# Kernel optimization log

Measured on AMD Instinct MI355X. Metric: run time of the kernel, lower is better.

The kernel has to match this reference:

```python
import jax, jax.numpy as jnp
import numpy as np

DIM = 1024; H = 16; KVH = 4; HD = 64          # head_dim = DIM // H
I = 2048                                       # intermediate_size = 2*DIM
N = 16                                         # ssm_state_size
DTR = 64                                       # dt_rank = DIM // 16
K = 4                                          # conv kernel
BASE = 10000.0
EPS = 1.1920929e-07                            # torch F.rms_norm default eps (fp32 finfo eps)

def rms_norm(x):
    return x * jax.lax.rsqrt(jnp.mean(x * x, axis=-1, keepdims=True) + EPS)

def rope_tables(S, dims):
    inv = 1.0 / BASE ** (jnp.arange(0, dims, 2, dtype=jnp.float32) / dims)
    f = jnp.outer(jnp.arange(S, dtype=jnp.float32), inv)   # [S, dims//2]
    return jnp.cos(f), jnp.sin(f)

def apply_rope(x, cos, sin):
    half = x.shape[-1] // 2
    x1, x2 = x[..., :half], x[..., half:]
    return jnp.concatenate([x1 * cos + x2 * sin, -x1 * sin + x2 * cos], axis=-1)

def setup_inputs() -> dict:
    key = jax.random.key(0)
    ks = jax.random.split(key, 12)
    B, S = 2, 2048
    def w(k, shape, s=0.02):
        return jax.random.normal(k, shape, jnp.float32) * s
    return {
        "x": jax.random.normal(ks[0], (B, S, DIM), jnp.float32),
        "W_mamba": w(ks[1], (2 * I, DIM)),
        "W_q": w(ks[2], (DIM, DIM)),
        "W_kv": w(ks[3], (2 * KVH * HD, DIM)),
        "q_gain": jnp.full((H,), 1.0, jnp.float32),
        "conv_w": w(ks[4], (I, K), 0.2),
        "conv_b": jnp.zeros((I,), jnp.float32),
        "W_xproj": w(ks[5], (DTR + 2 * N, I)),
        "W_dt": w(ks[6], (I, DTR)),
        "b_dt": w(ks[7], (I,), 0.5),
        "A_log": jnp.log(jnp.broadcast_to(jnp.arange(1, N + 1, dtype=jnp.float32), (I, N))),
        "D": jnp.ones((I,), jnp.float32),
        "W_mamba_out": w(ks[8], (DIM, I)),
        "W_proj": w(ks[9], (DIM, DIM)),
        "merge_alpha": jnp.zeros((1,), jnp.float32),
    }

def reference(x, W_mamba, W_q, W_kv, q_gain, conv_w, conv_b, W_xproj, W_dt, b_dt,
              A_log, D, W_mamba_out, W_proj, merge_alpha):
    B, S, _ = x.shape
    # --- parallel input projection for the mamba branch ---
    mp = x @ W_mamba.T                         # [B,S,2I]
    x_ssm, gate = mp[..., :I], mp[..., I:]
    # --- attention branch (GQA + full RoPE + per-head q gain) ---
    q = (x @ W_q.T).reshape(B, S, H, HD).transpose(0, 2, 1, 3)
    kv = x @ W_kv.T
    k = kv[..., :KVH * HD].reshape(B, S, KVH, HD).transpose(0, 2, 1, 3)
    v = kv[..., KVH * HD:].reshape(B, S, KVH, HD).transpose(0, 2, 1, 3)
    q = rms_norm(q); k = rms_norm(k)
    cos, sin = rope_tables(S, HD)
    q = apply_rope(q, cos, sin)
    k = apply_rope(k, cos, sin)
    q = q * q_gain[None, :, None, None]
    nrep = H // KVH
    k = jnp.repeat(k, nrep, axis=1)
    v = jnp.repeat(v, nrep, axis=1)
    scores = jnp.einsum('bhqd,bhkd->bhqk', q, k) / jnp.sqrt(jnp.float32(HD))
    mask = jnp.tril(jnp.ones((S, S), bool))
    scores = jnp.where(mask, scores, -jnp.inf)
    y = jnp.einsum('bhqk,bhkd->bhqd', jax.nn.softmax(scores, axis=-1), v)
    attn_out = y.transpose(0, 2, 1, 3).reshape(B, S, DIM)
    # --- mamba/SSM branch: causal depthwise conv1d + silu ---
    xc = x_ssm.transpose(0, 2, 1)              # [B,I,S]
    u = jax.lax.conv_general_dilated(xc, conv_w[:, None, :], (1,), [(K - 1, 0)],
                                     dimension_numbers=('NCH', 'OIH', 'NCH'),
                                     feature_group_count=I) + conv_b[None, :, None]
    u = u * jax.nn.sigmoid(u)                  # silu, [B,I,S]
    u_bsi = u.transpose(0, 2, 1)               # [B,S,I]
    params = u_bsi @ W_xproj.T                 # [B,S,DTR+2N]
    dt_low = params[..., :DTR]
    Bm = params[..., DTR:DTR + N]
    Cm = params[..., DTR + N:]
    delta = jax.nn.softplus(dt_low @ W_dt.T + b_dt)   # [B,S,I] (delta_bias + softplus)
    A = -jnp.exp(A_log)                        # [I,N]
    def step(state, inp):
        d_t, b_t, c_t, u_t = inp               # [B,I],[B,N],[B,N],[B,I]
        dA = jnp.exp(d_t[:, :, None] * A[None])
        state = state * dA + d_t[:, :, None] * b_t[:, None, :] * u_t[:, :, None]
        y_t = jnp.sum(state * c_t[:, None, :], axis=-1)
        return state, y_t
    xs = (delta.transpose(1, 0, 2), Bm.transpose(1, 0, 2),
          Cm.transpose(1, 0, 2), u_bsi.transpose(1, 0, 2))
    state0 = jnp.zeros((B, I, N), x.dtype)
    _, ys = jax.lax.scan(step, state0, xs)     # ys: [S,B,I]
    y_ssm = ys.transpose(1, 0, 2) + u_bsi * D  # + D skip
    y_ssm = y_ssm * (gate * jax.nn.sigmoid(gate))      # gated by silu(z)
    mamba_out = y_ssm @ W_mamba_out.T          # [B,S,DIM]
    # --- gated merge + output projection ---
    alpha = jax.nn.sigmoid(merge_alpha)
    merged = alpha * attn_out + (1.0 - alpha) * mamba_out
    return merged @ W_proj.T
```

## Files before the change

kernel.cpp:

```cpp
#include <hip/hip_runtime.h>
#include <hip/hip_bf16.h>

#define B_   2
#define S_   2048
#define T_   4096
#define DIM_ 1024
#define H_   16
#define KVH_ 4
#define HD_  64
#define I_   2048
#define N_   16
#define DTR_ 64
#define MB   ((size_t)1 << 20)

typedef __hip_bfloat16 bf16;
typedef __attribute__((ext_vector_type(8))) short short8;
typedef __attribute__((ext_vector_type(4))) short short4v;
typedef __attribute__((ext_vector_type(4))) float f32x4;

__device__ __forceinline__ float b2f(bf16 v){ return __bfloat162float(v); }
__device__ __forceinline__ bf16  f2b(float v){ return __float2bfloat16(v); }
__device__ __forceinline__ float s2f(short s){
  return __builtin_bit_cast(float, ((unsigned int)(unsigned short)s) << 16);
}
__device__ __forceinline__ short f2s(float v){
  return (short)__builtin_bit_cast(unsigned short, f2b(v));
}

__device__ __forceinline__ void async16(const void* g, void* l) {
  __builtin_amdgcn_global_load_lds((__attribute__((address_space(1))) void*)g,
                                   (__attribute__((address_space(3))) void*)l, 16, 0, 0);
}

__global__ __launch_bounds__(256)
void cast_f2b(const float* __restrict__ in, bf16* __restrict__ out, int n4)
{
  const int i = blockIdx.x * 256 + threadIdx.x;
  if (i >= n4) return;
  const float4 v = ((const float4*)in)[i];
  short4v o;
  o.x = f2s(v.x); o.y = f2s(v.y); o.z = f2s(v.z); o.w = f2s(v.w);
  *(short4v*)(out + (size_t)i * 4) = o;
}

template<int MODE, int TS>
__global__ __launch_bounds__(256)
void gemm_nt(const bf16* __restrict__ A, int lda,
             const bf16* __restrict__ W, int ldw,
             void* __restrict__ C, int ldc,
             bf16* __restrict__ Ct, int ldt,
             const float* __restrict__ bias,
             int M, int N, int K)
{
  __shared__ __align__(16) bf16 As[128*32];
  __shared__ __align__(16) bf16 Bs[128*32];
  const int tid  = threadIdx.x;
  const int lane = tid & 63;
  const int wave = tid >> 6;
  const int l16  = lane & 15;
  const int quad = lane >> 4;
  const int wm   = (wave >> 1) << 6;
  const int wn   = (wave & 1) << 6;
  const int m0   = blockIdx.x << 7;
  const int n0   = blockIdx.y << 7;

  f32x4 acc[4][4];
  const f32x4 zero = {0.f, 0.f, 0.f, 0.f};
  #pragma unroll
  for (int i = 0; i < 4; i++)
    #pragma unroll
    for (int j = 0; j < 4; j++) acc[i][j] = zero;

  for (int k0 = 0; k0 < K; k0 += 32) {
    #pragma unroll
    for (int p = 0; p < 2; p++) {
      const int linear = ((p << 8) + tid) << 4;
      const int row    = linear >> 6;
      const int inrow  = linear & 63;
      async16(A + (size_t)(m0 + row) * lda + k0 + (inrow >> 1), (char*)As + linear);
      int wr = n0 + row; if (wr > N - 1) wr = N - 1;
      async16(W + (size_t)wr * ldw + k0 + (inrow >> 1), (char*)Bs + linear);
    }
    __syncthreads();
    short8 af[4], bfr[4];
    #pragma unroll
    for (int mt = 0; mt < 4; mt++)
      af[mt] = *(const short8*)((const char*)As + ((wm + (mt << 4) + l16) << 6) + (quad << 4));
    #pragma unroll
    for (int nt = 0; nt < 4; nt++)
      bfr[nt] = *(const short8*)((const char*)Bs + ((wn + (nt << 4) + l16) << 6) + (quad << 4));
    #pragma unroll
    for (int mt = 0; mt < 4; mt++)
      #pragma unroll
      for (int nt = 0; nt < 4; nt++)
        acc[mt][nt] = __builtin_amdgcn_mfma_f32_16x16x32_bf16(af[mt], bfr[nt], acc[mt][nt], 0, 0, 0);
    __syncthreads();
  }

  #pragma unroll
  for (int mt = 0; mt < 4; mt++) {
    #pragma unroll
    for (int nt = 0; nt < 4; nt++) {
      const int col = n0 + wn + (nt << 4) + l16;
      if (col >= N) continue;
      const int rowbase = m0 + wm + (mt << 4) + (quad << 2);
      float v[4];
      #pragma unroll
      for (int r = 0; r < 4; r++) {
        float t = acc[mt][nt][r];
        if (MODE == 2) {
          t += bias[col];
          t = (t > 20.f) ? t : log1pf(__expf(t));
        }
        v[r] = t;
      }
      if (TS == 0 || TS == 2) {
        #pragma unroll
        for (int r = 0; r < 4; r++) {
          if (MODE == 0) ((float*)C)[(size_t)(rowbase + r) * ldc + col] = v[r];
          else           ((bf16*)C)[(size_t)(rowbase + r) * ldc + col] = f2b(v[r]);
        }
      }
      if (TS >= 1) {
        short4v p;
        #pragma unroll
        for (int r = 0; r < 4; r++) p[r] = f2s(v[r]);
        *(short4v*)(Ct + (size_t)col * ldt + rowbase) = p;
      }
    }
  }
}

__global__ __launch_bounds__(256)
void qkv_prep(const bf16* __restrict__ qraw, const bf16* __restrict__ kvraw,
              const float* __restrict__ q_gain,
              bf16* __restrict__ qn, bf16* __restrict__ kn, bf16* __restrict__ vt)
{
  const int wid  = blockIdx.x * 4 + (threadIdx.x >> 6);
  const int lane = threadIdx.x & 63;
  const int t    = wid / 24;
  const int slot = wid % 24;
  const int b = t >> 11, s = t & 2047;

  float val;
  if (slot < 16)       val = b2f(qraw [(size_t)t * 1024 + slot * 64 + lane]);
  else if (slot < 20)  val = b2f(kvraw[(size_t)t * 512  + (slot - 16) * 64 + lane]);
  else                 val = b2f(kvraw[(size_t)t * 512  + 256 + (slot - 20) * 64 + lane]);

  if (slot < 20) {
    float ss = val * val;
    #pragma unroll
    for (int off = 32; off; off >>= 1) ss += __shfl_xor(ss, off);
    val *= rsqrtf(ss * (1.0f / 64.0f) + 1.1920929e-07f);
    const int j = lane & 31;
    const float x1 = __shfl(val, j);
    const float x2 = __shfl(val, j + 32);
    const float inv = powf(10000.0f, -(float)j * (1.0f / 32.0f));
    const float ang = (float)s * inv;
    const float c = cosf(ang), sn = sinf(ang);
    val = (lane < 32) ? (x1 * c + x2 * sn) : (x2 * c - x1 * sn);
  }
  if (slot < 16) {
    val *= q_gain[slot];
    qn[((size_t)(b * 16 + slot) * 2048 + s) * 64 + lane] = f2b(val);
  } else if (slot < 20) {
    kn[((size_t)(b * 4 + (slot - 16)) * 2048 + s) * 64 + lane] = f2b(val);
  } else {
    vt[((size_t)(b * 4 + (slot - 20)) * 64 + lane) * 2048 + s] = f2b(val);
  }
}

__global__ __launch_bounds__(64)
void attn_fwd(const bf16* __restrict__ qn, const bf16* __restrict__ kn,
              const bf16* __restrict__ vt, bf16* __restrict__ attn)
{
  __shared__ __align__(16) bf16 Plds[16][72];
  const int b = blockIdx.z, h = blockIdx.y;
  const int lane = threadIdx.x;
  const int l16 = lane & 15, quad = lane >> 4;
  const int q0 = (127 - blockIdx.x) * 16;
  const int kvh = h >> 2;
  const bf16* Q  = qn + (size_t)(b * 16 + h)  * 2048 * 64;
  const bf16* Kp = kn + (size_t)(b * 4 + kvh) * 2048 * 64;
  const bf16* Vt = vt + (size_t)(b * 4 + kvh) * 64 * 2048;

  const short8 qf0 = *(const short8*)(Q + (size_t)(q0 + l16) * 64 + quad * 8);
  const short8 qf1 = *(const short8*)(Q + (size_t)(q0 + l16) * 64 + 32 + quad * 8);

  f32x4 acc[4];
  const f32x4 zero = {0.f, 0.f, 0.f, 0.f};
  #pragma unroll
  for (int i = 0; i < 4; i++) acc[i] = zero;
  float m_r[4], l_r[4];
  #pragma unroll
  for (int r = 0; r < 4; r++) { m_r[r] = -1e30f; l_r[r] = 0.f; }

  const int kend = q0 + 16;
  for (int kb = 0; kb < kend; kb += 64) {
    f32x4 s[4];
    #pragma unroll
    for (int t = 0; t < 4; t++) {
      const bf16* kr = Kp + (size_t)(kb + t * 16 + l16) * 64;
      const short8 kf0 = *(const short8*)(kr + quad * 8);
      const short8 kf1 = *(const short8*)(kr + 32 + quad * 8);
      f32x4 sv = zero;
      sv = __builtin_amdgcn_mfma_f32_16x16x32_bf16(qf0, kf0, sv, 0, 0, 0);
      sv = __builtin_amdgcn_mfma_f32_16x16x32_bf16(qf1, kf1, sv, 0, 0, 0);
      s[t] = sv;
    }
    float alpha[4], p[4][4];
    #pragma unroll
    for (int r = 0; r < 4; r++) {
      const int row = q0 + quad * 4 + r;
      float v[4];
      #pragma unroll
      for (int t = 0; t < 4; t++) {
        float x = s[t][r] * 0.125f;
        if (kb + t * 16 + l16 > row) x = -1e30f;
        v[t] = x;
      }
      float tm = fmaxf(fmaxf(v[0], v[1]), fmaxf(v[2], v[3]));
      tm = fmaxf(tm, __shfl_xor(tm, 1)); tm = fmaxf(tm, __shfl_xor(tm, 2));
      tm = fmaxf(tm, __shfl_xor(tm, 4)); tm = fmaxf(tm, __shfl_xor(tm, 8));
      const float nm = fmaxf(m_r[r], tm);
      alpha[r] = __expf(m_r[r] - nm);
      m_r[r] = nm;
      float ps = 0.f;
      #pragma unroll
      for (int t = 0; t < 4; t++) { p[r][t] = __expf(v[t] - nm); ps += p[r][t]; }
      ps += __shfl_xor(ps, 1); ps += __shfl_xor(ps, 2);
      ps += __shfl_xor(ps, 4); ps += __shfl_xor(ps, 8);
      l_r[r] = l_r[r] * alpha[r] + ps;
    }
    #pragma unroll
    for (int nt = 0; nt < 4; nt++)
      #pragma unroll
      for (int r = 0; r < 4; r++) acc[nt][r] *= alpha[r];

    #pragma unroll
    for (int r = 0; r < 4; r++)
      #pragma unroll
      for (int t = 0; t < 4; t++)
        Plds[quad * 4 + r][t * 16 + l16] = f2b(p[r][t]);

    #pragma unroll
    for (int c = 0; c < 2; c++) {
      const short8 pf = *(const short8*)(&Plds[l16][c * 32 + quad * 8]);
      #pragma unroll
      for (int nt = 0; nt < 4; nt++) {
        const short8 vf = *(const short8*)(Vt + (size_t)(nt * 16 + l16) * 2048 + kb + c * 32 + quad * 8);
        acc[nt] = __builtin_amdgcn_mfma_f32_16x16x32_bf16(pf, vf, acc[nt], 0, 0, 0);
      }
    }
  }

  #pragma unroll
  for (int nt = 0; nt < 4; nt++)
    #pragma unroll
    for (int r = 0; r < 4; r++) {
      const int row = q0 + quad * 4 + r;
      attn[((size_t)b * 2048 + row) * 1024 + h * 64 + nt * 16 + l16] = f2b(acc[nt][r] / l_r[r]);
    }
}

__global__ __launch_bounds__(256)
void conv_silu_t(const bf16* __restrict__ xssmT, const float* __restrict__ cw,
                 const float* __restrict__ cb, bf16* __restrict__ uT)
{
  const int i = blockIdx.x;
  const int t = blockIdx.y * 256 + threadIdx.x;
  const int s = t & 2047;
  float acc = cb[i];
  #pragma unroll
  for (int kk = 0; kk < 4; kk++) {
    if (s - 3 + kk >= 0)
      acc += s2f(__builtin_bit_cast(short, xssmT[(size_t)i * 4096 + t - 3 + kk])) * cw[i * 4 + kk];
  }
  const float sig = 1.f / (1.f + __expf(-acc));
  uT[(size_t)i * 4096 + t] = f2b(acc * sig);
}

__global__ __launch_bounds__(256)
void transpose_bf16(const bf16* __restrict__ in, bf16* __restrict__ out,
                    int R, int C)
{
  __shared__ bf16 tile[64][65];
  const int c0 = blockIdx.x * 64, r0 = blockIdx.y * 64;
  #pragma unroll
  for (int it = 0; it < 2; it++) {
    const int linear = (it * 256 + threadIdx.x) * 8;
    const int r = linear >> 6, cc = linear & 63;
    const short8 v = *(const short8*)(in + (size_t)(r0 + r) * C + c0 + cc);
    #pragma unroll
    for (int k = 0; k < 8; k++)
      tile[r][cc + k] = __builtin_bit_cast(bf16, (unsigned short)v[k]);
  }
  __syncthreads();
  #pragma unroll
  for (int it = 0; it < 2; it++) {
    const int linear = (it * 256 + threadIdx.x) * 8;
    const int oc = linear >> 6, k = linear & 63;
    short8 v;
    #pragma unroll
    for (int kk = 0; kk < 8; kk++)
      v[kk] = (short)__builtin_bit_cast(unsigned short, tile[k + kk][oc]);
    *(short8*)(out + (size_t)(c0 + oc) * R + r0 + k) = v;
  }
}

__global__ __launch_bounds__(256)
void finish_y(const bf16* __restrict__ yT, const bf16* __restrict__ gT,
              bf16* __restrict__ out)
{
  __shared__ bf16 tile[64][65];
  const int t0 = blockIdx.x * 64, i0 = blockIdx.y * 64;
  #pragma unroll
  for (int it = 0; it < 2; it++) {
    const int linear = (it * 256 + threadIdx.x) * 8;
    const int r = linear >> 6, cc = linear & 63;
    const size_t off = (size_t)(i0 + r) * 4096 + t0 + cc;
    const short8 y8 = *(const short8*)(yT + off);
    const short8 g8 = *(const short8*)(gT + off);
    #pragma unroll
    for (int k = 0; k < 8; k++) {
      const float g  = s2f(g8[k]);
      const float gs = g / (1.f + __expf(-g));
      tile[r][cc + k] = f2b(s2f(y8[k]) * gs);
    }
  }
  __syncthreads();
  #pragma unroll
  for (int it = 0; it < 2; it++) {
    const int linear = (it * 256 + threadIdx.x) * 8;
    const int oc = linear >> 6, k = linear & 63;
    short8 v;
    #pragma unroll
    for (int kk = 0; kk < 8; kk++)
      v[kk] = (short)__builtin_bit_cast(unsigned short, tile[k + kk][oc]);
    *(short8*)(out + (size_t)(t0 + oc) * 2048 + i0 + k) = v;
  }
}

__global__ __launch_bounds__(256)
void ssm_scan(const bf16* __restrict__ dltT, const bf16* __restrict__ uT,
              const bf16* __restrict__ prmT, const float* __restrict__ A_log,
              const float* __restrict__ Dv, bf16* __restrict__ youtT)
{
  __shared__ float Pl[16][17], Fl[16][17], Il[16][17];
  const int blk = blockIdx.x;
  const int b = blk >> 11, i = blk & 2047;
  const int n = threadIdx.x & 15, c = threadIdx.x >> 4;
  const float a  = -__expf(A_log[i * 16 + n]);
  const float Di = Dv[i];
  const size_t rowoff = (size_t)b * 2048 + c * 128;
  const bf16* dp = dltT  + (size_t)i * 4096 + rowoff;
  const bf16* up = uT    + (size_t)i * 4096 + rowoff;
  const bf16* Bp = prmT  + (size_t)(64 + n) * 4096 + rowoff;
  const bf16* Cp = prmT  + (size_t)(80 + n) * 4096 + rowoff;
  bf16*       yp = youtT + (size_t)i * 4096 + rowoff;

  float P = 1.f, F = 0.f;
  for (int j0 = 0; j0 < 128; j0 += 8) {
    const short8 d8 = *(const short8*)(dp + j0);
    const short8 u8 = *(const short8*)(up + j0);
    const short8 B8 = *(const short8*)(Bp + j0);
    #pragma unroll
    for (int j = 0; j < 8; j++) {
      const float dt = s2f(d8[j]);
      const float dA = __expf(dt * a);
      P *= dA;
      F = F * dA + dt * s2f(u8[j]) * s2f(B8[j]);
    }
  }
  Pl[n][c] = P; Fl[n][c] = F;
  __syncthreads();

  if (threadIdx.x < 16) {
    const int nn = threadIdx.x;
    float s = 0.f;
    #pragma unroll
    for (int cc = 0; cc < 16; cc++) {
      Il[nn][cc] = s;
      s = Fl[nn][cc] + Pl[nn][cc] * s;
    }
  }
  __syncthreads();

  float state = Il[n][c];
  for (int j0 = 0; j0 < 128; j0 += 8) {
    const short8 d8 = *(const short8*)(dp + j0);
    const short8 u8 = *(const short8*)(up + j0);
    const short8 B8 = *(const short8*)(Bp + j0);
    const short8 C8 = *(const short8*)(Cp + j0);
    short8 o8;
    #pragma unroll
    for (int j = 0; j < 8; j++) {
      const float dt = s2f(d8[j]);
      const float ut = s2f(u8[j]);
      const float dA = __expf(dt * a);
      state = state * dA + dt * ut * s2f(B8[j]);
      float y = state * s2f(C8[j]);
      y += __shfl_xor(y, 1); y += __shfl_xor(y, 2);
      y += __shfl_xor(y, 4); y += __shfl_xor(y, 8);
      o8[j] = f2s(y + ut * Di);
    }
    if (n == 0) *(short8*)(yp + j0) = o8;
  }
}

__global__ __launch_bounds__(256)
void merge_k(const bf16* __restrict__ attn, const bf16* __restrict__ mamba,
             const float* __restrict__ malpha, bf16* __restrict__ merged)
{
  const size_t idx = (size_t)blockIdx.x * 256 + threadIdx.x;
  const float al = 1.f / (1.f + __expf(-malpha[0]));
  merged[idx] = f2b(al * b2f(attn[idx]) + (1.f - al) * b2f(mamba[idx]));
}

extern "C" void kernel_launch(void* const* d_in, const int* in_sizes, int n_in,
                              void* d_out, int out_size, void* d_ws, size_t ws_size,
                              hipStream_t stream)
{
  const float* x_f     = (const float*)d_in[0];
  const float* Wm_f    = (const float*)d_in[1];
  const float* Wq_f    = (const float*)d_in[2];
  const float* Wkv_f   = (const float*)d_in[3];
  const float* q_gain  = (const float*)d_in[4];
  const float* conv_w  = (const float*)d_in[5];
  const float* conv_b  = (const float*)d_in[6];
  const float* Wxp_f   = (const float*)d_in[7];
  const float* Wdt_f   = (const float*)d_in[8];
  const float* b_dt    = (const float*)d_in[9];
  const float* A_log   = (const float*)d_in[10];
  const float* Dv      = (const float*)d_in[11];
  const float* Wmo_f   = (const float*)d_in[12];
  const float* Wp_f    = (const float*)d_in[13];
  const float* malpha  = (const float*)d_in[14];

  char* wp = (char*)d_ws;
  bf16*  xb    = (bf16*)(wp + 0 * MB);
  bf16*  Wm_b  = (bf16*)(wp + 8 * MB);
  bf16*  Wq_b  = (bf16*)(wp + 16 * MB);
  bf16*  Wkv_b = (bf16*)(wp + 18 * MB);
  bf16*  xssmT = (bf16*)(wp + 19 * MB);
  bf16*  gateT = (bf16*)(wp + 35 * MB);
  bf16*  u     = (bf16*)(wp + 51 * MB);
  bf16*  uT    = (bf16*)(wp + 67 * MB);
  bf16*  qraw  = (bf16*)(wp + 83 * MB);
  bf16*  kvraw = (bf16*)(wp + 91 * MB);
  bf16*  dltT  = (bf16*)(wp + 95 * MB);
  bf16*  qn    = (bf16*)(wp + 0 * MB);
  bf16*  kn    = (bf16*)(wp + 8 * MB);
  bf16*  vtb   = (bf16*)(wp + 10 * MB);
  bf16*  Wxp_b = (bf16*)(wp + 12 * MB);
  bf16*  Wdt_b = (bf16*)(wp + 12 * MB + 512 * 1024);
  bf16*  prm   = (bf16*)(wp + 13 * MB);
  bf16*  prmT  = (bf16*)(wp + 13 * MB + 768 * 1024);
  bf16*  Wp_b  = (bf16*)(wp + 16 * MB);
  bf16*  attnb = (bf16*)(wp + 83 * MB);
  bf16*  Wmo_b = (bf16*)(wp + 91 * MB);
  bf16*  ybuf  = (bf16*)(wp + 19 * MB);
  bf16*  ybufT = (bf16*)(wp + 51 * MB);
  bf16*  mam   = (bf16*)(wp + 35 * MB);
  bf16*  mrg   = (bf16*)(wp + 43 * MB);
  (void)ws_size; (void)in_sizes; (void)n_in; (void)out_size;

  auto cast = [&](const float* src, bf16* dst, int n) {
    const int n4 = n >> 2;
    cast_f2b<<<dim3((n4 + 255) / 256), 256, 0, stream>>>(src, dst, n4);
  };
  cast(x_f,   xb,    T_ * 1024);
  cast(Wm_f,  Wm_b,  4096 * 1024);
  cast(Wq_f,  Wq_b,  1024 * 1024);
  cast(Wkv_f, Wkv_b, 512 * 1024);

  gemm_nt<1,1><<<dim3(32, 16), 256, 0, stream>>>(xb, 1024, Wm_b,               1024, nullptr, 0, xssmT, 4096, nullptr, T_, 2048, 1024);
  gemm_nt<1,1><<<dim3(32, 16), 256, 0, stream>>>(xb, 1024, Wm_b + 2048 * 1024, 1024, nullptr, 0, gateT, 4096, nullptr, T_, 2048, 1024);
  gemm_nt<1,0><<<dim3(32, 8),  256, 0, stream>>>(xb, 1024, Wq_b,  1024, qraw,  1024, nullptr, 0, nullptr, T_, 1024, 1024);
  gemm_nt<1,0><<<dim3(32, 4),  256, 0, stream>>>(xb, 1024, Wkv_b, 1024, kvraw,  512, nullptr, 0, nullptr, T_,  512, 1024);

  qkv_prep<<<dim3((T_ * 24) / 4), 256, 0, stream>>>(qraw, kvraw, q_gain, qn, kn, vtb);
  conv_silu_t<<<dim3(2048, 16), 256, 0, stream>>>(xssmT, conv_w, conv_b, uT);
  attn_fwd<<<dim3(128, 16, 2), 64, 0, stream>>>(qn, kn, vtb, attnb);
  transpose_bf16<<<dim3(64, 32), 256, 0, stream>>>(uT, u, 2048, 4096);

  cast(Wxp_f, Wxp_b, 96 * 2048);
  cast(Wdt_f, Wdt_b, 2048 * 64);
  cast(Wmo_f, Wmo_b, 1024 * 2048);
  cast(Wp_f,  Wp_b,  1024 * 1024);

  gemm_nt<1,2><<<dim3(32, 1),  256, 0, stream>>>(u, 2048, Wxp_b, 2048, prm, 96, prmT, 4096, nullptr, T_, 96, 2048);
  gemm_nt<2,1><<<dim3(32, 16), 256, 0, stream>>>(prm, 96, Wdt_b, 64, nullptr, 0, dltT, 4096, b_dt, T_, 2048, 64);
  ssm_scan<<<dim3(4096), 256, 0, stream>>>(dltT, uT, prmT, A_log, Dv, ybufT);
  finish_y<<<dim3(64, 32), 256, 0, stream>>>(ybufT, gateT, ybuf);
  gemm_nt<1,0><<<dim3(32, 8),  256, 0, stream>>>(ybuf, 2048, Wmo_b, 2048, mam, 1024, nullptr, 0, nullptr, T_, 1024, 2048);

  merge_k<<<dim3(16384), 256, 0, stream>>>(attnb, mam, malpha, mrg);
  gemm_nt<0,0><<<dim3(32, 8),  256, 0, stream>>>(mrg, 1024, Wp_b, 1024, (float*)d_out, 1024, nullptr, 0, nullptr, T_, 1024, 1024);
}
```

Measured before the change: 900.4 us.

## Replace online softmax with fixed max bound and MFMA row-sum

The attention kernel no longer tracks a running row max or rescales its accumulators. It subtracts a static upper bound, 8*|q_gain|+1, which holds because q and k are RMS-normalized. Row sums are taken with an extra MFMA against a vector of bf16 ones instead of cross-lane shuffle reductions. This drops the shuffle chains, the per-block exp of alpha and the accumulator rescaling, at the risk of exp underflow when gains are large or scores sit far below the bound.

```diff
diff --git a/kernel.cpp b/kernel.cpp
--- a/kernel.cpp
+++ b/kernel.cpp
@@ -172,7 +172,8 @@
 
 __global__ __launch_bounds__(64)
 void attn_fwd(const bf16* __restrict__ qn, const bf16* __restrict__ kn,
-              const bf16* __restrict__ vt, bf16* __restrict__ attn)
+              const bf16* __restrict__ vt, const float* __restrict__ q_gain,
+              bf16* __restrict__ attn)
 {
   __shared__ __align__(16) bf16 Plds[16][72];
   const int b = blockIdx.z, h = blockIdx.y;
@@ -183,17 +184,19 @@
   const bf16* Q  = qn + (size_t)(b * 16 + h)  * 2048 * 64;
   const bf16* Kp = kn + (size_t)(b * 4 + kvh) * 2048 * 64;
   const bf16* Vt = vt + (size_t)(b * 4 + kvh) * 64 * 2048;
+  const float M = 8.0f * fabsf(q_gain[h]) + 1.0f;
 
   const short8 qf0 = *(const short8*)(Q + (size_t)(q0 + l16) * 64 + quad * 8);
   const short8 qf1 = *(const short8*)(Q + (size_t)(q0 + l16) * 64 + 32 + quad * 8);
 
+  const short one_bf = (short)0x3F80;
+  const short8 ones = {one_bf, one_bf, one_bf, one_bf, one_bf, one_bf, one_bf, one_bf};
+
   f32x4 acc[4];
   const f32x4 zero = {0.f, 0.f, 0.f, 0.f};
   #pragma unroll
   for (int i = 0; i < 4; i++) acc[i] = zero;
-  float m_r[4], l_r[4];
-  #pragma unroll
-  for (int r = 0; r < 4; r++) { m_r[r] = -1e30f; l_r[r] = 0.f; }
+  f32x4 accl = zero;
 
   const int kend = q0 + 16;
   for (int kb = 0; kb < kend; kb += 64) {
@@ -208,41 +211,16 @@
       sv = __builtin_amdgcn_mfma_f32_16x16x32_bf16(qf1, kf1, sv, 0, 0, 0);
       s[t] = sv;
     }
-    float alpha[4], p[4][4];
     #pragma unroll
     for (int r = 0; r < 4; r++) {
       const int row = q0 + quad * 4 + r;
-      float v[4];
       #pragma unroll
       for (int t = 0; t < 4; t++) {
-        float x = s[t][r] * 0.125f;
-        if (kb + t * 16 + l16 > row) x = -1e30f;
-        v[t] = x;
+        const float p = (kb + t * 16 + l16 > row) ? 0.f
+                        : __expf(s[t][r] * 0.125f - M);
+        Plds[quad * 4 + r][t * 16 + l16] = f2b(p);
       }
-      float tm = fmaxf(fmaxf(v[0], v[1]), fmaxf(v[2], v[3]));
-      tm = fmaxf(tm, __shfl_xor(tm, 1)); tm = fmaxf(tm, __shfl_xor(tm, 2));
-      tm = fmaxf(tm, __shfl_xor(tm, 4)); tm = fmaxf(tm, __shfl_xor(tm, 8));
-      const float nm = fmaxf(m_r[r], tm);
-      alpha[r] = __expf(m_r[r] - nm);
-      m_r[r] = nm;
-      float ps = 0.f;
-      #pragma unroll
-      for (int t = 0; t < 4; t++) { p[r][t] = __expf(v[t] - nm); ps += p[r][t]; }
-      ps += __shfl_xor(ps, 1); ps += __shfl_xor(ps, 2);
-      ps += __shfl_xor(ps, 4); ps += __shfl_xor(ps, 8);
-      l_r[r] = l_r[r] * alpha[r] + ps;
-    }
-    #pragma unroll
-    for (int nt = 0; nt < 4; nt++)
-      #pragma unroll
-      for (int r = 0; r < 4; r++) acc[nt][r] *= alpha[r];
-
-    #pragma unroll
-    for (int r = 0; r < 4; r++)
-      #pragma unroll
-      for (int t = 0; t < 4; t++)
-        Plds[quad * 4 + r][t * 16 + l16] = f2b(p[r][t]);
-
+    }
     #pragma unroll
     for (int c = 0; c < 2; c++) {
       const short8 pf = *(const short8*)(&Plds[l16][c * 32 + quad * 8]);
@@ -251,16 +229,18 @@
         const short8 vf = *(const short8*)(Vt + (size_t)(nt * 16 + l16) * 2048 + kb + c * 32 + quad * 8);
         acc[nt] = __builtin_amdgcn_mfma_f32_16x16x32_bf16(pf, vf, acc[nt], 0, 0, 0);
       }
-    }
-  }
-
-  #pragma unroll
-  for (int nt = 0; nt < 4; nt++)
-    #pragma unroll
-    for (int r = 0; r < 4; r++) {
-      const int row = q0 + quad * 4 + r;
-      attn[((size_t)b * 2048 + row) * 1024 + h * 64 + nt * 16 + l16] = f2b(acc[nt][r] / l_r[r]);
-    }
+      accl = __builtin_amdgcn_mfma_f32_16x16x32_bf16(pf, ones, accl, 0, 0, 0);
+    }
+  }
+
+  #pragma unroll
+  for (int r = 0; r < 4; r++) {
+    const float rl = 1.0f / accl[r];
+    const int row = q0 + quad * 4 + r;
+    #pragma unroll
+    for (int nt = 0; nt < 4; nt++)
+      attn[((size_t)b * 2048 + row) * 1024 + h * 64 + nt * 16 + l16] = f2b(acc[nt][r] * rl);
+  }
 }
 
 __global__ __launch_bounds__(256)
@@ -481,7 +461,7 @@
 
   qkv_prep<<<dim3((T_ * 24) / 4), 256, 0, stream>>>(qraw, kvraw, q_gain, qn, kn, vtb);
   conv_silu_t<<<dim3(2048, 16), 256, 0, stream>>>(xssmT, conv_w, conv_b, uT);
-  attn_fwd<<<dim3(128, 16, 2), 64, 0, stream>>>(qn, kn, vtb, attnb);
+  attn_fwd<<<dim3(128, 16, 2), 64, 0, stream>>>(qn, kn, vtb, q_gain, attnb);
   transpose_bf16<<<dim3(64, 32), 256, 0, stream>>>(uT, u, 2048, 4096);
 
   cast(Wxp_f, Wxp_b, 96 * 2048);
```

Measured after the change: 901.9 us. About the same (+0.2%).
